# Optimization experiments

Hardware: AMD Instinct MI355X
Metric: run time of the kernel (lower is better)

The kernel has to match this reference:

```python
import jax, jax.numpy as jnp
import numpy as np

B = 131072   # batch (tokens)
D = 512      # d_model
P = 10       # n_programs
H = D // 4   # extractor hidden
MAXO = 4     # max operands
MAXR = 3     # max results


def setup_inputs() -> dict:
    key = jax.random.key(0)
    ks = jax.random.split(key, 6)
    hidden = jax.random.normal(ks[0], (B, D), jnp.float32)
    program_ids = jax.random.randint(ks[1], (B,), 0, P)
    Wr = jax.random.normal(ks[2], (D, P), jnp.float32) * (1.0 / np.sqrt(D))
    br = jnp.zeros((P,), jnp.float32)
    # stacked per-program extractor MLPs, output padded to MAXO (extra cols unused)
    W1 = jax.random.normal(ks[3], (P, D, H), jnp.float32) * (1.0 / np.sqrt(D))
    b1 = jnp.zeros((P, H), jnp.float32)
    W2 = jax.random.normal(ks[4], (P, H, MAXO), jnp.float32) * (1.0 / np.sqrt(H))
    b2 = jnp.zeros((P, MAXO), jnp.float32)
    return {"hidden": hidden, "program_ids": program_ids, "Wr": Wr, "br": br,
            "W1": W1, "b1": b1, "W2": W2, "b2": b2}


def _time_decompose(total_minutes):
    days = jnp.floor(total_minutes / 1440.0)
    rem = total_minutes - days * 1440.0
    hours = jnp.floor(rem / 60.0)
    minutes = rem - hours * 60.0
    return hours, minutes, days


def _safe(b):
    # avoid NaN/Inf from zero denominators in Mod/FloorDiv
    return jnp.where(b == 0, 1.0, b)


def _programs():
    # (fn -> tuple of result arrays, n_operands), order matches DEFAULT_PROGRAMS
    return [
        (lambda a, b: (a + b,), 2),                                   # IntAdd
        (lambda a, b: (a - b,), 2),                                   # IntSub
        (lambda a, b: (a * b,), 2),                                   # IntMul
        (lambda a, b: (jnp.mod(a, _safe(b)),), 2),                    # Mod
        (lambda a, b: (jnp.floor(a / _safe(b)),), 2),                 # FloorDiv
        (lambda h1, m1, h2, m2: _time_decompose(h1 * 60 + m1 + h2 * 60 + m2), 4),          # TimeAdd
        (lambda h1, m1, h2, m2: _time_decompose(h1 * 60 + m1 - (h2 * 60 + m2)), 4),        # TimeSub
        (lambda h1, m1, h2, m2: _time_decompose(jnp.abs(h1 * 60 + m1 - (h2 * 60 + m2))), 4),  # DurationBetween
        (lambda a, b: ((a > b).astype(jnp.float32),), 2),             # Greater
        (lambda a, b: ((a == b).astype(jnp.float32),), 2),            # Equal
    ]


def _compute_results(ops_rounded):
    # ops_rounded: [P, B, MAXO] -> results_all [P, B, MAXR]
    outs = []
    for idx, (fn, nop) in enumerate(_programs()):
        args = [ops_rounded[idx, :, i] for i in range(nop)]
        res = fn(*args)
        cols = list(res) + [jnp.zeros_like(res[0])] * (MAXR - len(res))
        outs.append(jnp.stack(cols, axis=-1))  # [B, MAXR]
    return jnp.stack(outs, axis=0)  # [P, B, MAXR]


def reference(hidden, program_ids, Wr, br, W1, b1, W2, b2):
    router_logits = hidden @ Wr + br                                  # [B, P]
    pre = jnp.einsum('bd,pdh->pbh', hidden, W1) + b1[:, None, :]      # [P, B, H]
    ops = jnp.einsum('pbh,pho->pbo', jax.nn.gelu(pre, approximate=False), W2) + b2[:, None, :]  # [P, B, MAXO]
    ops_rounded = jnp.round(ops)  # round_ste forward = round
    results_all = _compute_results(ops_rounded)                       # [P, B, MAXR]
    # combine: each row takes the result of its own program (masked scatter in torch)
    results = results_all[program_ids, jnp.arange(hidden.shape[0])]   # [B, MAXR]
    results = jax.lax.stop_gradient(results)  # torch .detach()
    return results, router_logits, ops, program_ids
```

## Files before the change

### kernel.cpp

```cpp
#include <hip/hip_runtime.h>
#include <math.h>

constexpr int D_   = 512;
constexpr int H_   = 128;
constexpr int P_   = 10;
constexpr int MAXO = 4;
constexpr int BM   = 128;
constexpr int BK   = 32;

typedef _Float16 f16;
typedef f16 f16x4 __attribute__((ext_vector_type(4)));
typedef f16 f16x8 __attribute__((ext_vector_type(8)));
typedef float f32x4 __attribute__((ext_vector_type(4)));

__device__ __forceinline__ float gelu_exact(float x) {
    return 0.5f * x * (1.0f + erff(x * 0.70710678118654752f));
}

__device__ __forceinline__ void time_decomp(float t, float& hr, float& mi, float& dy) {
    float days = floorf(t / 1440.0f);
    float rem  = t - days * 1440.0f;
    float hours = floorf(rem / 60.0f);
    float minutes = rem - hours * 60.0f;
    hr = hours; mi = minutes; dy = days;
}

__device__ __forceinline__ void g2l16(const f16* g, f16* l) {
    __builtin_amdgcn_global_load_lds(
        (const __attribute__((address_space(1))) void*)g,
        (__attribute__((address_space(3))) void*)l, 16, 0, 0);
}

__global__ __launch_bounds__(256) void cvt_w1_kernel(
    const float* __restrict__ W1, f16* __restrict__ hi, f16* __restrict__ lo)
{
    int i = blockIdx.x * 256 + threadIdx.x;
    float x = W1[i];
    f16 h = (f16)x;
    f16 L = (f16)(x - (float)h);
    int dh = i % (D_ * H_);
    int p  = i / (D_ * H_);
    int d  = dh / H_;
    int hh = dh % H_;
    size_t o = ((size_t)(p * H_ + hh)) * D_ + d;
    hi[o] = h; lo[o] = L;
}

__global__ __launch_bounds__(256) void cvt_hidden_kernel(
    const float* __restrict__ hidden, f16* __restrict__ hi, f16* __restrict__ lo)
{
    size_t i = ((size_t)blockIdx.x * 256 + threadIdx.x) * 8;
    f32x4 v0 = *(const f32x4*)(hidden + i);
    f32x4 v1 = *(const f32x4*)(hidden + i + 4);
    f16x8 vh, vl;
#pragma unroll
    for (int j = 0; j < 4; ++j) {
        f16 h0 = (f16)v0[j]; vh[j] = h0; vl[j] = (f16)(v0[j] - (float)h0);
        f16 h1 = (f16)v1[j]; vh[j + 4] = h1; vl[j + 4] = (f16)(v1[j] - (float)h1);
    }
    *(f16x8*)(hi + i) = vh;
    *(f16x8*)(lo + i) = vl;
}

template <bool PRECONV>
__global__ __launch_bounds__(256) void extractor_kernel(
    const float* __restrict__ hidden,
    const f16*   __restrict__ hidHi,
    const f16*   __restrict__ hidLo,
    const int*   __restrict__ pids,
    const f16*   __restrict__ W1Thi,
    const f16*   __restrict__ W1Tlo,
    const float* __restrict__ b1,
    const float* __restrict__ W2,
    const float* __restrict__ b2,
    float* __restrict__ out_results,
    float* __restrict__ out_ops,
    int B)
{
    __shared__ __align__(16) char smem[71680];
    f16* A0h = (f16*)(smem);
    f16* A0l = (f16*)(smem + 8192);
    f16* B0h = (f16*)(smem + 16384);
    f16* B0l = (f16*)(smem + 24576);
    f16* A1h = (f16*)(smem + 32768);
    f16* A1l = (f16*)(smem + 40960);
    f16* B1h = (f16*)(smem + 49152);
    f16* B1l = (f16*)(smem + 57344);
    float* red = (float*)(smem + 65536);
    float* W2s = (float*)(smem + 69632);

    const int bid = blockIdx.x;
    const int ngroups = gridDim.x / P_;
    int g, p;
    if ((ngroups & 7) == 0) {
        const int gpx = ngroups >> 3;
        const int x   = bid & 7;
        const int q   = bid >> 3;
        g = x * gpx + q / P_;
        p = q % P_;
    } else {
        g = bid / P_;
        p = bid % P_;
    }
    const int b0  = g * BM;
    const int tid = threadIdx.x;
    const int l   = tid & 63;
    const int w   = tid >> 6;
    const int wm  = w >> 1, wn = w & 1;
    const int l15 = l & 15, l4 = l >> 4;

    if (tid < H_) {
        ((f32x4*)W2s)[tid] = ((const f32x4*)(W2 + (size_t)p * H_ * 4))[tid];
    }

    f32x4 acc[4][4];
#pragma unroll
    for (int mi = 0; mi < 4; ++mi)
#pragma unroll
        for (int ni = 0; ni < 4; ++ni) acc[mi][ni] = (f32x4){0.f, 0.f, 0.f, 0.f};

    const f16* Bhig = W1Thi + (size_t)p * H_ * D_;
    const f16* Blog = W1Tlo + (size_t)p * H_ * D_;

    auto stageB = [&](int kc, f16* Bh, f16* Bl) {
#pragma unroll
        for (int t = 0; t < 2; ++t) {
            int h0 = w * 32 + t * 16;
            size_t go = (size_t)(h0 + (l >> 2)) * D_ + kc * BK + (l & 3) * 8;
            g2l16(Bhig + go, Bh + h0 * BK);
            g2l16(Blog + go, Bl + h0 * BK);
        }
    };
    auto stageA = [&](int kc, f16* Ah, f16* Al) {
        if constexpr (PRECONV) {
#pragma unroll
            for (int t = 0; t < 2; ++t) {
                int m0 = w * 32 + t * 16;
                size_t ga = (size_t)(b0 + m0 + (l >> 2)) * D_ + kc * BK + (l & 3) * 8;
                g2l16(hidHi + ga, Ah + m0 * BK);
                g2l16(hidLo + ga, Al + m0 * BK);
            }
        } else {
#pragma unroll
            for (int it = 0; it < 4; ++it) {
                int i  = tid + it * 256;
                int m  = i >> 3;
                int k4 = (i & 7) * 4;
                f32x4 v = *(const f32x4*)(hidden + (size_t)(b0 + m) * D_ + kc * BK + k4);
                f16x4 vh, vl;
#pragma unroll
                for (int j = 0; j < 4; ++j) {
                    f16 hj = (f16)v[j];
                    vh[j] = hj;
                    vl[j] = (f16)(v[j] - (float)hj);
                }
                *(f16x4*)&Ah[m * BK + k4] = vh;
                *(f16x4*)&Al[m * BK + k4] = vl;
            }
        }
    };
    auto compute = [&](const f16* Ah, const f16* Al, const f16* Bh, const f16* Bl) {
        f16x8 bh[4], bl[4];
#pragma unroll
        for (int ni = 0; ni < 4; ++ni) {
            int hrow = wn * 64 + ni * 16 + l15;
            bh[ni] = *(const f16x8*)&Bh[hrow * BK + l4 * 8];
            bl[ni] = *(const f16x8*)&Bl[hrow * BK + l4 * 8];
        }
#pragma unroll
        for (int mi = 0; mi < 4; ++mi) {
            int mrow = wm * 64 + mi * 16 + l15;
            f16x8 a_h = *(const f16x8*)&Ah[mrow * BK + l4 * 8];
            f16x8 a_l = *(const f16x8*)&Al[mrow * BK + l4 * 8];
#pragma unroll
            for (int ni = 0; ni < 4; ++ni) {
                acc[mi][ni] = __builtin_amdgcn_mfma_f32_16x16x32_f16(a_l, bh[ni], acc[mi][ni], 0, 0, 0);
                acc[mi][ni] = __builtin_amdgcn_mfma_f32_16x16x32_f16(a_h, bl[ni], acc[mi][ni], 0, 0, 0);
                acc[mi][ni] = __builtin_amdgcn_mfma_f32_16x16x32_f16(a_h, bh[ni], acc[mi][ni], 0, 0, 0);
            }
        }
    };

    stageA(0, A0h, A0l);
    stageB(0, B0h, B0l);
    __syncthreads();
    for (int kc = 0; kc < 16; kc += 2) {
        stageA(kc + 1, A1h, A1l);
        stageB(kc + 1, B1h, B1l);
        compute(A0h, A0l, B0h, B0l);
        __syncthreads();
        if (kc + 2 < 16) {
            stageA(kc + 2, A0h, A0l);
            stageB(kc + 2, B0h, B0l);
        }
        compute(A1h, A1l, B1h, B1l);
        __syncthreads();
    }

    float b1v[4];
#pragma unroll
    for (int ni = 0; ni < 4; ++ni)
        b1v[ni] = b1[p * H_ + wn * 64 + ni * 16 + l15];

#pragma unroll
    for (int mi = 0; mi < 4; ++mi) {
        float po[4][4];
#pragma unroll
        for (int r = 0; r < 4; ++r)
#pragma unroll
            for (int o = 0; o < 4; ++o) po[r][o] = 0.0f;

#pragma unroll
        for (int ni = 0; ni < 4; ++ni) {
            int h = wn * 64 + ni * 16 + l15;
            f32x4 w4 = ((const f32x4*)W2s)[h];
#pragma unroll
            for (int r = 0; r < 4; ++r) {
                float gg = gelu_exact(acc[mi][ni][r] + b1v[ni]);
#pragma unroll
                for (int o = 0; o < 4; ++o) po[r][o] = fmaf(gg, w4[o], po[r][o]);
            }
        }
#pragma unroll
        for (int off = 1; off < 16; off <<= 1) {
#pragma unroll
            for (int r = 0; r < 4; ++r)
#pragma unroll
                for (int o = 0; o < 4; ++o)
                    po[r][o] += __shfl_xor(po[r][o], off, 64);
        }
        float v = po[0][0];
#pragma unroll
        for (int rr = 0; rr < 4; ++rr)
#pragma unroll
            for (int oo = 0; oo < 4; ++oo)
                if (l15 == rr * 4 + oo) v = po[rr][oo];
        red[(wn * 128 + wm * 64 + mi * 16 + l4 * 4 + (l15 >> 2)) * 4 + (l15 & 3)] = v;
    }
    __syncthreads();

    if (tid < BM) {
        int b = b0 + tid;
        const float* r0p = &red[(0 * 128 + tid) * 4];
        const float* r1p = &red[(1 * 128 + tid) * 4];
        float o0 = r0p[0] + r1p[0] + b2[p * 4 + 0];
        float o1 = r0p[1] + r1p[1] + b2[p * 4 + 1];
        float o2 = r0p[2] + r1p[2] + b2[p * 4 + 2];
        float o3 = r0p[3] + r1p[3] + b2[p * 4 + 3];
        *reinterpret_cast<float4*>(out_ops + ((size_t)p * B + b) * MAXO) =
            make_float4(o0, o1, o2, o3);

        if (pids[b] == p) {
            float a0 = rintf(o0), a1 = rintf(o1), a2 = rintf(o2), a3 = rintf(o3);
            float r0 = 0.0f, r1 = 0.0f, r2 = 0.0f;
            switch (p) {
                case 0: r0 = a0 + a1; break;
                case 1: r0 = a0 - a1; break;
                case 2: r0 = a0 * a1; break;
                case 3: {
                    float bs = (a1 == 0.0f) ? 1.0f : a1;
                    float m = fmodf(a0, bs);
                    if (m != 0.0f && ((m < 0.0f) != (bs < 0.0f))) m += bs;
                    r0 = m;
                } break;
                case 4: {
                    float bs = (a1 == 0.0f) ? 1.0f : a1;
                    r0 = floorf(a0 / bs);
                } break;
                case 5: { float tt = a0 * 60.0f + a1 + a2 * 60.0f + a3; time_decomp(tt, r0, r1, r2); } break;
                case 6: { float tt = a0 * 60.0f + a1 - (a2 * 60.0f + a3); time_decomp(tt, r0, r1, r2); } break;
                case 7: { float tt = fabsf(a0 * 60.0f + a1 - (a2 * 60.0f + a3)); time_decomp(tt, r0, r1, r2); } break;
                case 8: r0 = (a0 > a1) ? 1.0f : 0.0f; break;
                case 9: r0 = (a0 == a1) ? 1.0f : 0.0f; break;
            }
            size_t ob = (size_t)b * 3;
            out_results[ob + 0] = r0;
            out_results[ob + 1] = r1;
            out_results[ob + 2] = r2;
        }
    }
}

__global__ __launch_bounds__(256) void router_kernel(
    const float* __restrict__ hidden, const float* __restrict__ Wr,
    const float* __restrict__ br, const int* __restrict__ pids,
    float* __restrict__ out_router, float* __restrict__ out_pids, int B)
{
    __shared__ float Wrs[D_ * 12];
    const int tid = threadIdx.x;
    for (int i = tid; i < D_ * P_; i += 256) {
        int k = i / P_;
        int q = i - k * P_;
        Wrs[k * 12 + q] = Wr[i];
    }
    __syncthreads();

    const int lane = tid & 63;
    const int wv   = tid >> 6;
    const int b    = blockIdx.x * 4 + wv;
    const float* hrow = hidden + (size_t)b * D_;

    float acc[P_];
#pragma unroll
    for (int q = 0; q < P_; ++q) acc[q] = 0.0f;

#pragma unroll
    for (int j = 0; j < 8; ++j) {
        int k = j * 64 + lane;
        float hv = hrow[k];
        float wv12[12];
        *reinterpret_cast<float4*>(&wv12[0]) = *reinterpret_cast<const float4*>(&Wrs[k * 12 + 0]);
        *reinterpret_cast<float4*>(&wv12[4]) = *reinterpret_cast<const float4*>(&Wrs[k * 12 + 4]);
        *reinterpret_cast<float2*>(&wv12[8]) = *reinterpret_cast<const float2*>(&Wrs[k * 12 + 8]);
#pragma unroll
        for (int q = 0; q < P_; ++q) acc[q] = fmaf(hv, wv12[q], acc[q]);
    }

#pragma unroll
    for (int off = 1; off < 64; off <<= 1) {
#pragma unroll
        for (int q = 0; q < P_; ++q)
            acc[q] += __shfl_xor(acc[q], off, 64);
    }

    if (lane == 0) {
        float* o = out_router + (size_t)b * P_;
#pragma unroll
        for (int q = 0; q < P_; ++q) o[q] = acc[q] + br[q];
        out_pids[b] = (float)pids[b];
    }
}

extern "C" void kernel_launch(void* const* d_in, const int* in_sizes, int n_in,
                              void* d_out, int out_size, void* d_ws, size_t ws_size,
                              hipStream_t stream) {
    const float* hidden = (const float*)d_in[0];
    const int*   pids   = (const int*)  d_in[1];
    const float* Wr     = (const float*)d_in[2];
    const float* br     = (const float*)d_in[3];
    const float* W1     = (const float*)d_in[4];
    const float* b1     = (const float*)d_in[5];
    const float* W2     = (const float*)d_in[6];
    const float* b2     = (const float*)d_in[7];

    const int B = in_sizes[1];

    float* out         = (float*)d_out;
    float* out_results = out;
    float* out_router  = out + (size_t)B * 3;
    float* out_ops     = out + (size_t)B * 13;
    float* out_pids    = out + (size_t)B * 13 + (size_t)P_ * B * MAXO;

    const size_t nW1  = (size_t)P_ * H_ * D_;
    const size_t nHid = (size_t)B * D_;
    const size_t need = (2 * nW1 + 2 * nHid) * sizeof(f16);

    f16* W1Thi = (f16*)d_ws;
    f16* W1Tlo = W1Thi + nW1;

    cvt_w1_kernel<<<(int)(nW1 / 256), 256, 0, stream>>>(W1, W1Thi, W1Tlo);

    if (ws_size >= need) {
        f16* hidHi = W1Tlo + nW1;
        f16* hidLo = hidHi + nHid;
        cvt_hidden_kernel<<<(int)(nHid / (256 * 8)), 256, 0, stream>>>(hidden, hidHi, hidLo);
        extractor_kernel<true><<<(B / BM) * P_, 256, 0, stream>>>(
            hidden, hidHi, hidLo, pids, W1Thi, W1Tlo, b1, W2, b2,
            out_results, out_ops, B);
    } else {
        extractor_kernel<false><<<(B / BM) * P_, 256, 0, stream>>>(
            hidden, nullptr, nullptr, pids, W1Thi, W1Tlo, b1, W2, b2,
            out_results, out_ops, B);
    }

    router_kernel<<<B / 4, 256, 0, stream>>>(hidden, Wr, br, pids,
                                             out_router, out_pids, B);
}
```

Baseline: 883.6 us.

## Fuse router with hidden fp16 split and swizzle GEMM LDS layout

Merges the hidden-to-fp16 hi/lo conversion into the router kernel so hidden is read once for both, removing a separate pass over the large activation tensor. Applies an XOR swizzle to the LDS tile layout for A and B staging and reads, to reduce bank conflicts in the MFMA operand loads. Adds launch_bounds occupancy hint of 2 blocks per CU. The fused kernel writes fp16 with scalar 2-byte stores per lane, which may coalesce less well than the old vectorized conversion.

```diff
diff --git a/kernel.cpp b/kernel.cpp
--- a/kernel.cpp
+++ b/kernel.cpp
@@ -46,24 +46,65 @@
     hi[o] = h; lo[o] = L;
 }
 
-__global__ __launch_bounds__(256) void cvt_hidden_kernel(
-    const float* __restrict__ hidden, f16* __restrict__ hi, f16* __restrict__ lo)
+template <bool WRITE_SPLIT>
+__global__ __launch_bounds__(256) void router_cvt_kernel(
+    const float* __restrict__ hidden, const float* __restrict__ Wr,
+    const float* __restrict__ br, const int* __restrict__ pids,
+    float* __restrict__ out_router, float* __restrict__ out_pids,
+    f16* __restrict__ hidHi, f16* __restrict__ hidLo, int B)
 {
-    size_t i = ((size_t)blockIdx.x * 256 + threadIdx.x) * 8;
-    f32x4 v0 = *(const f32x4*)(hidden + i);
-    f32x4 v1 = *(const f32x4*)(hidden + i + 4);
-    f16x8 vh, vl;
-#pragma unroll
-    for (int j = 0; j < 4; ++j) {
-        f16 h0 = (f16)v0[j]; vh[j] = h0; vl[j] = (f16)(v0[j] - (float)h0);
-        f16 h1 = (f16)v1[j]; vh[j + 4] = h1; vl[j + 4] = (f16)(v1[j] - (float)h1);
-    }
-    *(f16x8*)(hi + i) = vh;
-    *(f16x8*)(lo + i) = vl;
+    __shared__ float Wrs[D_ * 12];
+    const int tid = threadIdx.x;
+    for (int i = tid; i < D_ * P_; i += 256) {
+        int k = i / P_;
+        int q = i - k * P_;
+        Wrs[k * 12 + q] = Wr[i];
+    }
+    __syncthreads();
+
+    const int lane = tid & 63;
+    const int wv   = tid >> 6;
+    const int b    = blockIdx.x * 4 + wv;
+    const float* hrow = hidden + (size_t)b * D_;
+
+    float acc[P_];
+#pragma unroll
+    for (int q = 0; q < P_; ++q) acc[q] = 0.0f;
+
+#pragma unroll
+    for (int j = 0; j < 8; ++j) {
+        int k = j * 64 + lane;
+        float hv = hrow[k];
+        if (WRITE_SPLIT) {
+            f16 hh = (f16)hv;
+            hidHi[(size_t)b * D_ + k] = hh;
+            hidLo[(size_t)b * D_ + k] = (f16)(hv - (float)hh);
+        }
+        float wv12[12];
+        *reinterpret_cast<float4*>(&wv12[0]) = *reinterpret_cast<const float4*>(&Wrs[k * 12 + 0]);
+        *reinterpret_cast<float4*>(&wv12[4]) = *reinterpret_cast<const float4*>(&Wrs[k * 12 + 4]);
+        *reinterpret_cast<float2*>(&wv12[8]) = *reinterpret_cast<const float2*>(&Wrs[k * 12 + 8]);
+#pragma unroll
+        for (int q = 0; q < P_; ++q) acc[q] = fmaf(hv, wv12[q], acc[q]);
+    }
+
+#pragma unroll
+    for (int off = 1; off < 64; off <<= 1) {
+#pragma unroll
+        for (int q = 0; q < P_; ++q)
+            acc[q] += __shfl_xor(acc[q], off, 64);
+    }
+
+    if (lane == 0) {
+        float* o = out_router + (size_t)b * P_;
+#pragma unroll
+        for (int q = 0; q < P_; ++q) o[q] = acc[q] + br[q];
+        out_pids[b] = (float)pids[b];
+    }
 }
 
 template <bool PRECONV>
-__global__ __launch_bounds__(256) void extractor_kernel(
+__global__ __launch_bounds__(256, 2) void extractor_kernel(
     const float* __restrict__ hidden,
     const f16*   __restrict__ hidHi,
     const f16*   __restrict__ hidLo,
@@ -78,14 +119,6 @@
     int B)
 {
     __shared__ __align__(16) char smem[71680];
-    f16* A0h = (f16*)(smem);
-    f16* A0l = (f16*)(smem + 8192);
-    f16* B0h = (f16*)(smem + 16384);
-    f16* B0l = (f16*)(smem + 24576);
-    f16* A1h = (f16*)(smem + 32768);
-    f16* A1l = (f16*)(smem + 40960);
-    f16* B1h = (f16*)(smem + 49152);
-    f16* B1l = (f16*)(smem + 57344);
     float* red = (float*)(smem + 65536);
     float* W2s = (float*)(smem + 69632);
 
@@ -109,6 +142,9 @@
     const int wm  = w >> 1, wn = w & 1;
     const int l15 = l & 15, l4 = l >> 4;
 
+    const int sg8 = (((l & 3) ^ ((l >> 3) & 3))) * 8;
+    const int rd8 = ((l4 ^ ((l15 >> 1) & 3))) * 8;
+
     if (tid < H_) {
         ((f32x4*)W2s)[tid] = ((const f32x4*)(W2 + (size_t)p * H_ * 4))[tid];
     }
@@ -122,21 +158,25 @@
     const f16* Bhig = W1Thi + (size_t)p * H_ * D_;
     const f16* Blog = W1Tlo + (size_t)p * H_ * D_;
 
-    auto stageB = [&](int kc, f16* Bh, f16* Bl) {
+    auto stageB = [&](int kc, char* buf) {
+        f16* Bh = (f16*)(buf + 16384);
+        f16* Bl = (f16*)(buf + 24576);
 #pragma unroll
         for (int t = 0; t < 2; ++t) {
             int h0 = w * 32 + t * 16;
-            size_t go = (size_t)(h0 + (l >> 2)) * D_ + kc * BK + (l & 3) * 8;
+            size_t go = (size_t)(h0 + (l >> 2)) * D_ + kc * BK + sg8;
             g2l16(Bhig + go, Bh + h0 * BK);
             g2l16(Blog + go, Bl + h0 * BK);
         }
     };
-    auto stageA = [&](int kc, f16* Ah, f16* Al) {
+    auto stageA = [&](int kc, char* buf) {
+        f16* Ah = (f16*)(buf);
+        f16* Al = (f16*)(buf + 8192);
         if constexpr (PRECONV) {
 #pragma unroll
             for (int t = 0; t < 2; ++t) {
                 int m0 = w * 32 + t * 16;
-                size_t ga = (size_t)(b0 + m0 + (l >> 2)) * D_ + kc * BK + (l & 3) * 8;
+                size_t ga = (size_t)(b0 + m0 + (l >> 2)) * D_ + kc * BK + sg8;
                 g2l16(hidHi + ga, Ah + m0 * BK);
                 g2l16(hidLo + ga, Al + m0 * BK);
             }
@@ -146,6 +186,7 @@
                 int i  = tid + it * 256;
                 int m  = i >> 3;
                 int k4 = (i & 7) * 4;
+                int ks = ((k4 >> 3) ^ ((m >> 1) & 3)) * 8 + (k4 & 7);
                 f32x4 v = *(const f32x4*)(hidden + (size_t)(b0 + m) * D_ + kc * BK + k4);
                 f16x4 vh, vl;
 #pragma unroll
@@ -154,24 +195,28 @@
                     vh[j] = hj;
                     vl[j] = (f16)(v[j] - (float)hj);
                 }
-                *(f16x4*)&Ah[m * BK + k4] = vh;
-                *(f16x4*)&Al[m * BK + k4] = vl;
+                *(f16x4*)&Ah[m * BK + ks] = vh;
+                *(f16x4*)&Al[m * BK + ks] = vl;
             }
         }
     };
-    auto compute = [&](const f16* Ah, const f16* Al, const f16* Bh, const f16* Bl) {
+    auto compute = [&](const char* buf) {
+        const f16* Ah = (const f16*)(buf);
+        const f16* Al = (const f16*)(buf + 8192);
+        const f16* Bh = (const f16*)(buf + 16384);
+        const f16* Bl = (const f16*)(buf + 24576);
         f16x8 bh[4], bl[4];
 #pragma unroll
         for (int ni = 0; ni < 4; ++ni) {
             int hrow = wn * 64 + ni * 16 + l15;
-            bh[ni] = *(const f16x8*)&Bh[hrow * BK + l4 * 8];
-            bl[ni] = *(const f16x8*)&Bl[hrow * BK + l4 * 8];
+            bh[ni] = *(const f16x8*)&Bh[hrow * BK + rd8];
+            bl[ni] = *(const f16x8*)&Bl[hrow * BK + rd8];
         }
 #pragma unroll
         for (int mi = 0; mi < 4; ++mi) {
             int mrow = wm * 64 + mi * 16 + l15;
-            f16x8 a_h = *(const f16x8*)&Ah[mrow * BK + l4 * 8];
-            f16x8 a_l = *(const f16x8*)&Al[mrow * BK + l4 * 8];
+            f16x8 a_h = *(const f16x8*)&Ah[mrow * BK + rd8];
+            f16x8 a_l = *(const f16x8*)&Al[mrow * BK + rd8];
 #pragma unroll
             for (int ni = 0; ni < 4; ++ni) {
                 acc[mi][ni] = __builtin_amdgcn_mfma_f32_16x16x32_f16(a_l, bh[ni], acc[mi][ni], 0, 0, 0);
@@ -181,19 +226,22 @@
         }
     };
 
-    stageA(0, A0h, A0l);
-    stageB(0, B0h, B0l);
+    char* buf0 = smem;
+    char* buf1 = smem + 32768;
+
+    stageA(0, buf0);
+    stageB(0, buf0);
     __syncthreads();
     for (int kc = 0; kc < 16; kc += 2) {
-        stageA(kc + 1, A1h, A1l);
-        stageB(kc + 1, B1h, B1l);
-        compute(A0h, A0l, B0h, B0l);
+        stageA(kc + 1, buf1);
+        stageB(kc + 1, buf1);
+        compute(buf0);
         __syncthreads();
         if (kc + 2 < 16) {
-            stageA(kc + 2, A0h, A0l);
-            stageB(kc + 2, B0h, B0l);
-        }
-        compute(A1h, A1l, B1h, B1l);
+            stageA(kc + 2, buf0);
+            stageB(kc + 2, buf0);
+        }
+        compute(buf1);
         __syncthreads();
     }
 
@@ -281,56 +329,6 @@
     }
 }
 
-__global__ __launch_bounds__(256) void router_kernel(
-    const float* __restrict__ hidden, const float* __restrict__ Wr,
-    const float* __restrict__ br, const int* __restrict__ pids,
-    float* __restrict__ out_router, float* __restrict__ out_pids, int B)
-{
-    __shared__ float Wrs[D_ * 12];
-    const int tid = threadIdx.x;
-    for (int i = tid; i < D_ * P_; i += 256) {
-        int k = i / P_;
-        int q = i - k * P_;
-        Wrs[k * 12 + q] = Wr[i];
-    }
-    __syncthreads();
-
-    const int lane = tid & 63;
-    const int wv   = tid >> 6;
-    const int b    = blockIdx.x * 4 + wv;
-    const float* hrow = hidden + (size_t)b * D_;
-
-    float acc[P_];
-#pragma unroll
-    for (int q = 0; q < P_; ++q) acc[q] = 0.0f;
-
-#pragma unroll
-    for (int j = 0; j < 8; ++j) {
-        int k = j * 64 + lane;
-        float hv = hrow[k];
-        float wv12[12];
-        *reinterpret_cast<float4*>(&wv12[0]) = *reinterpret_cast<const float4*>(&Wrs[k * 12 + 0]);
-        *reinterpret_cast<float4*>(&wv12[4]) = *reinterpret_cast<const float4*>(&Wrs[k * 12 + 4]);
-        *reinterpret_cast<float2*>(&wv12[8]) = *reinterpret_cast<const float2*>(&Wrs[k * 12 + 8]);
-#pragma unroll
-        for (int q = 0; q < P_; ++q) acc[q] = fmaf(hv, wv12[q], acc[q]);
-    }
-
-#pragma unroll
-    for (int off = 1; off < 64; off <<= 1) {
-#pragma unroll
-        for (int q = 0; q < P_; ++q)
-            acc[q] += __shfl_xor(acc[q], off, 64);
-    }
-
-    if (lane == 0) {
-        float* o = out_router + (size_t)b * P_;
-#pragma unroll
-        for (int q = 0; q < P_; ++q) o[q] = acc[q] + br[q];
-        out_pids[b] = (float)pids[b];
-    }
-}
-
 extern "C" void kernel_launch(void* const* d_in, const int* in_sizes, int n_in,
                               void* d_out, int out_size, void* d_ws, size_t ws_size,
                               hipStream_t stream) {
@@ -363,16 +361,16 @@
     if (ws_size >= need) {
         f16* hidHi = W1Tlo + nW1;
         f16* hidLo = hidHi + nHid;
-        cvt_hidden_kernel<<<(int)(nHid / (256 * 8)), 256, 0, stream>>>(hidden, hidHi, hidLo);
+        router_cvt_kernel<true><<<B / 4, 256, 0, stream>>>(
+            hidden, Wr, br, pids, out_router, out_pids, hidHi, hidLo, B);
         extractor_kernel<true><<<(B / BM) * P_, 256, 0, stream>>>(
             hidden, hidHi, hidLo, pids, W1Thi, W1Tlo, b1, W2, b2,
             out_results, out_ops, B);
     } else {
+        router_cvt_kernel<false><<<B / 4, 256, 0, stream>>>(
+            hidden, Wr, br, pids, out_router, out_pids, nullptr, nullptr, B);
         extractor_kernel<false><<<(B / BM) * P_, 256, 0, stream>>>(
             hidden, nullptr, nullptr, pids, W1Thi, W1Tlo, b1, W2, b2,
             out_results, out_ops, B);
     }
-
-    router_kernel<<<B / 4, 256, 0, stream>>>(hidden, Wr, br, pids,
-                                             out_router, out_pids, B);
-}
+}
```

Result: faster. 793.4 us (-10.2%).
